# Optimization experiments

Measured on AMD Instinct MI355X. Metric: run time of the kernel, lower is better.

## Reference

```python
import jax, jax.numpy as jnp
import numpy as np

N, K, P, C, H, E, Q, G = 50000, 8, 512, 64, 128, 1600000, 500000, 64

def _gelu(x):
    return jax.nn.gelu(x, approximate=False)  # torch F.gelu default = exact erf

def _mlp(x, Wi, bi, Wh, bh, Wo, bo, Wp=None, bp=None):
    # MLP: lin_in -> gelu -> hid -> (proj skip if in>hidden) -> skip+gelu -> lin_out
    skip = x if Wp is None else x @ Wp.T + bp
    h = _gelu(x @ Wi.T + bi)
    h = h @ Wh.T + bh
    return (skip + _gelu(h)) @ Wo.T + bo

def _sage(x, src, dst, Wl, bl, Wr, n):
    # PyG SAGEConv: mean-aggregate source features at dst, then lin_l(agg)+lin_r(x)
    s = jax.ops.segment_sum(x[src], dst, num_segments=n)
    cnt = jax.ops.segment_sum(jnp.ones((src.shape[0], 1), x.dtype), dst, num_segments=n)
    agg = s / jnp.maximum(cnt, 1.0)
    return agg @ Wl.T + bl + x @ Wr.T

def setup_inputs():
    key = jax.random.key(0)
    ks = iter(jax.random.split(key, 64))
    def lin(o, i):
        return (jax.random.normal(next(ks), (o, i), jnp.float32) / np.sqrt(i)).astype(jnp.float32)
    def bias(o):
        return jnp.zeros((o,), jnp.float32)
    inp = {}
    inp["x"] = jax.random.normal(next(ks), (N, K, P), jnp.float32)
    inp["batch"] = jnp.sort(jax.random.randint(next(ks), (N,), 0, G))
    inp["edge_index"] = jax.random.randint(next(ks), (2, E), 0, N)
    inp["src_idx"] = jax.random.randint(next(ks), (Q,), 0, N)
    inp["dst_idx"] = jax.random.randint(next(ks), (Q,), 0, N)
    # Embedder.mlp : MLP(P, P, H) with proj (P > H)
    inp.update(em_in_W=lin(H, P), em_in_b=bias(H), em_hid_W=lin(H, H), em_hid_b=bias(H),
               em_out_W=lin(P, H), em_out_b=bias(P), em_proj_W=lin(H, P), em_proj_b=bias(H))
    # Embedder.rho : MLP(P, C, H) with proj
    inp.update(rho_in_W=lin(H, P), rho_in_b=bias(H), rho_hid_W=lin(H, H), rho_hid_b=bias(H),
               rho_out_W=lin(C, H), rho_out_b=bias(C), rho_proj_W=lin(H, P), rho_proj_b=bias(H))
    for i in (1, 2, 3):
        inp[f"c{i}_ll_W"] = lin(C, C); inp[f"c{i}_ll_b"] = bias(C); inp[f"c{i}_lr_W"] = lin(C, C)
    # head MLP(3C, 2C, 2C) with proj (3C > 2C)
    inp.update(h1_in_W=lin(H, 3 * C), h1_in_b=bias(H), h1_hid_W=lin(H, H), h1_hid_b=bias(H),
               h1_out_W=lin(2 * C, H), h1_out_b=bias(2 * C), h1_proj_W=lin(H, 3 * C), h1_proj_b=bias(H))
    # head MLP(2C, 1, 2C), no proj
    inp.update(h2_in_W=lin(H, 2 * C), h2_in_b=bias(H), h2_hid_W=lin(H, H), h2_hid_b=bias(H),
               h2_out_W=lin(1, H), h2_out_b=bias(1))
    return inp

def reference(x, batch, edge_index, src_idx, dst_idx,
              em_in_W, em_in_b, em_hid_W, em_hid_b, em_out_W, em_out_b, em_proj_W, em_proj_b,
              rho_in_W, rho_in_b, rho_hid_W, rho_hid_b, rho_out_W, rho_out_b, rho_proj_W, rho_proj_b,
              c1_ll_W, c1_ll_b, c1_lr_W, c2_ll_W, c2_ll_b, c2_lr_W, c3_ll_W, c3_ll_b, c3_lr_W,
              h1_in_W, h1_in_b, h1_hid_W, h1_hid_b, h1_out_W, h1_out_b, h1_proj_W, h1_proj_b,
              h2_in_W, h2_in_b, h2_hid_W, h2_hid_b, h2_out_W, h2_out_b):
    n = x.shape[0]
    # Embedder: per-point MLP, gelu, sum over point-set dim, then rho (dropout = eval identity)
    h = _gelu(_mlp(x, em_in_W, em_in_b, em_hid_W, em_hid_b, em_out_W, em_out_b, em_proj_W, em_proj_b))
    z = _mlp(h.sum(-2), rho_in_W, rho_in_b, rho_hid_W, rho_hid_b, rho_out_W, rho_out_b, rho_proj_W, rho_proj_b)
    src, dst = edge_index[0], edge_index[1]
    z = z + _gelu(_sage(z, src, dst, c1_ll_W, c1_ll_b, c1_lr_W, n))
    z = z + _gelu(_sage(z, src, dst, c2_ll_W, c2_ll_b, c2_lr_W, n))
    z = z + _gelu(_sage(z, src, dst, c3_ll_W, c3_ll_b, c3_lr_W, n))
    node_embeddings = z
    # global_max_pool keyed by batch id, broadcast back via gather
    graph_emb = jax.ops.segment_max(z, batch, num_segments=G)
    ge = graph_emb[batch[src_idx]]  # == graph_emb[batch][src_idx]
    se, de = z[src_idx], z[dst_idx]
    xy = jnp.concatenate([se, de, ge], axis=-1)
    yx = jnp.concatenate([de, se, ge], axis=-1)
    def head(q):
        t = jax.nn.relu(_mlp(q, h1_in_W, h1_in_b, h1_hid_W, h1_hid_b, h1_out_W, h1_out_b, h1_proj_W, h1_proj_b))
        return _mlp(t, h2_in_W, h2_in_b, h2_hid_W, h2_hid_b, h2_out_W, h2_out_b)
    return (node_embeddings, (head(xy), head(yx)), xy)
```

## Files before the change

### kernel.cpp

```cpp
#include <hip/hip_runtime.h>

typedef unsigned short US;
typedef unsigned int   UI;
typedef short  short8 __attribute__((ext_vector_type(8)));
typedef US     u16x8  __attribute__((ext_vector_type(8)));
typedef float  f32x4  __attribute__((ext_vector_type(4)));

#define DEVI __device__ __forceinline__

DEVI float bf2f(US u){ UI i = ((UI)u) << 16; float f; __builtin_memcpy(&f, &i, 4); return f; }
DEVI US f2bf(float x){ UI i; __builtin_memcpy(&i, &x, 4); UI r = (i + 0x7FFFu + ((i >> 16) & 1u)) >> 16; return (US)r; }
DEVI float gelu_f(float x){
    float x2 = x * x;
    float m  = x * fmaf(x2, -0.1029432f, -2.3022052f);
    float e  = __builtin_amdgcn_exp2f(m);
    return x * __builtin_amdgcn_rcpf(1.0f + e);
}
DEVI UI encf(float f){ UI u; __builtin_memcpy(&u, &f, 4); return (u & 0x80000000u) ? ~u : (u | 0x80000000u); }
DEVI float decf(UI u){ UI b = (u & 0x80000000u) ? (u ^ 0x80000000u) : ~u; float f; __builtin_memcpy(&f, &b, 4); return f; }
DEVI int swz(int r, int c, int ld){ int i = r * ld + c; return i ^ ((r & 7) << 3); }

DEVI UI pkbf(float a, float b){ UI u; asm("v_cvt_pk_bf16_f32 %0, %1, %2" : "=v"(u) : "v"(a), "v"(b)); return u; }
DEVI void st4(US* T, int row, int col, float v0, float v1, float v2, float v3){
    uint2 p; p.x = pkbf(v0, v1); p.y = pkbf(v2, v3);
    *(uint2*)&T[swz(row, col, 256)] = p;
}
DEVI void ld4(const US* T, int row, int col, float& v0, float& v1, float& v2, float& v3){
    uint2 q = *(const uint2*)&T[swz(row, col, 256)];
    v0 = bf2f((US)(q.x & 0xffff)); v1 = bf2f((US)(q.x >> 16));
    v2 = bf2f((US)(q.y & 0xffff)); v3 = bf2f((US)(q.y >> 16));
}

enum : int { O_EmW1 = 0, O_EmWh = 131072, O_EmWo = 147456, O_RhoW1 = 212992,
             O_RhoWh = 344064, O_RhoWo = 360448, O_Cat1 = 368640, O_Cat2 = 376832,
             O_Cat3 = 385024, O_H1W1 = 393216, O_H1Wh = 442368, O_H1Wo = 458752,
             O_H2W1 = 475136, O_H2Wh = 491520, W_TOTAL = 507904 };

template<int NT, int NKC, int NTHR, bool SWAP = false>
DEVI void stageWD(const US* __restrict__ Wg, int Kw, const US* __restrict__ A, int lda,
                  int ab0, int ab1, int ab2, int arow0, US* Wb, int tid, f32x4 (&acc)[NT])
{
    const int lane = tid & 63;
    const int wc = (tid >> 6) & 1;
    constexpr int SLAB = NT * 32 * 64;
    #pragma unroll
    for (int n = 0; n < NT; ++n) acc[n] = (f32x4){0.f, 0.f, 0.f, 0.f};
    constexpr int J = (NT * 256) / NTHR;
    u16x8 wreg[J];
    #pragma unroll
    for (int j = 0; j < J; ++j) {
        const int c = tid + NTHR * j;
        wreg[j] = *(const u16x8*)(Wg + (size_t)(c >> 3) * Kw + (c & 7) * 8);
    }
    #pragma unroll
    for (int j = 0; j < J; ++j) {
        const int c = tid + NTHR * j;
        *(u16x8*)&Wb[swz(c >> 3, (c & 7) * 8, 64)] = wreg[j];
    }
    #pragma unroll
    for (int kc = 0; kc < NKC; ++kc) {
        __syncthreads();
        if (kc + 1 < NKC) {
            #pragma unroll
            for (int j = 0; j < J; ++j) {
                const int c = tid + NTHR * j;
                wreg[j] = *(const u16x8*)(Wg + (size_t)(c >> 3) * Kw + (kc + 1) * 64 + (c & 7) * 8);
            }
        }
        const int ab = (kc == 0) ? ab0 : ((kc == 1) ? ab1 : ab2);
        const int bufr = (kc & 1) * SLAB;
        #pragma unroll
        for (int sub = 0; sub < 2; ++sub) {
            const int kk = sub * 32 + ((lane >> 4) << 3);
            short8 a = *(const short8*)&A[swz(arow0 + (lane & 15), ab + kk, lda)];
            #pragma unroll
            for (int n = 0; n < NT; ++n) {
                short8 b = *(const short8*)&Wb[bufr + swz(wc * (NT * 16) + n * 16 + (lane & 15), kk, 64)];
                if (SWAP) acc[n] = __builtin_amdgcn_mfma_f32_16x16x32_bf16(b, a, acc[n], 0, 0, 0);
                else      acc[n] = __builtin_amdgcn_mfma_f32_16x16x32_bf16(a, b, acc[n], 0, 0, 0);
            }
        }
        if (kc + 1 < NKC) {
            const int bufw = ((kc + 1) & 1) * SLAB;
            #pragma unroll
            for (int j = 0; j < J; ++j) {
                const int c = tid + NTHR * j;
                *(u16x8*)&Wb[bufw + swz(c >> 3, (c & 7) * 8, 64)] = wreg[j];
            }
        }
    }
    __syncthreads();
}

template<int NT, int TOTC, int TOTCN, int NKC, bool LAST, bool SWAP>
DEVI void stageWC2(const US* __restrict__ Wg, int Kw, const US* __restrict__ nextWg, int nKw,
                   const US* __restrict__ A, int lda,
                   int aA0, int aA1, int aA2, int aB0, int aB1, int aB2,
                   int arowA, int rofB, int colb,
                   US* Wb, int off0, int off1, int wrN, int tid,
                   f32x4 (&accA)[NT], f32x4 (&accB)[NT])
{
    const int lane = tid & 63;
    const int l15 = lane & 15;
    const int h8 = (lane >> 4) << 3;
    #pragma unroll
    for (int n = 0; n < NT; ++n) {
        accA[n] = (f32x4){0.f, 0.f, 0.f, 0.f};
        accB[n] = (f32x4){0.f, 0.f, 0.f, 0.f};
    }
    constexpr int J  = TOTC  / 128;
    constexpr int JN = TOTCN / 128;
    constexpr int JM = (J > JN) ? J : JN;
    u16x8 wreg[JM];
    #pragma unroll
    for (int kc = 0; kc < NKC; ++kc) {
        __syncthreads();
        if (kc + 1 < NKC) {
            #pragma unroll
            for (int j = 0; j < J; ++j) {
                const int c = tid + 1024 * j;
                wreg[j] = *(const u16x8*)(Wg + (size_t)(c >> 3) * Kw + (kc + 1) * 64 + (c & 7) * 8);
            }
        } else if (!LAST) {
            #pragma unroll
            for (int j = 0; j < JN; ++j) {
                const int c = tid + 1024 * j;
                wreg[j] = *(const u16x8*)(nextWg + (size_t)(c >> 3) * nKw + (c & 7) * 8);
            }
        }
        const int abA = (kc == 0) ? aA0 : ((kc == 1) ? aA1 : aA2);
        const int abB = (kc == 0) ? aB0 : ((kc == 1) ? aB1 : aB2);
        const int rd = (kc & 1) ? off1 : off0;
        #pragma unroll
        for (int sub = 0; sub < 2; ++sub) {
            const int kk = sub * 32 + h8;
            short8 aA = *(const short8*)&A[swz(arowA + l15, abA + kk, lda)];
            short8 aB = *(const short8*)&A[swz(arowA + rofB + l15, abB + kk, lda)];
            #pragma unroll
            for (int n = 0; n < NT; ++n) {
                short8 b = *(const short8*)&Wb[rd + swz(colb + n * 16 + l15, kk, 64)];
                if (SWAP) {
                    accA[n] = __builtin_amdgcn_mfma_f32_16x16x32_bf16(b, aA, accA[n], 0, 0, 0);
                    accB[n] = __builtin_amdgcn_mfma_f32_16x16x32_bf16(b, aB, accB[n], 0, 0, 0);
                } else {
                    accA[n] = __builtin_amdgcn_mfma_f32_16x16x32_bf16(aA, b, accA[n], 0, 0, 0);
                    accB[n] = __builtin_amdgcn_mfma_f32_16x16x32_bf16(aB, b, accB[n], 0, 0, 0);
                }
            }
        }
        if (kc + 1 < NKC) {
            const int wr_ = (kc & 1) ? off0 : off1;
            #pragma unroll
            for (int j = 0; j < J; ++j) {
                const int c = tid + 1024 * j;
                *(u16x8*)&Wb[wr_ + swz(c >> 3, (c & 7) * 8, 64)] = wreg[j];
            }
        } else if (!LAST) {
            #pragma unroll
            for (int j = 0; j < JN; ++j) {
                const int c = tid + 1024 * j;
                *(u16x8*)&Wb[wrN + swz(c >> 3, (c & 7) * 8, 64)] = wreg[j];
            }
        }
    }
    __syncthreads();
}

template<int NT, int NTHR>
DEVI void preloadW(const US* __restrict__ Wg, int Kw, US* Wb, int off, int tid)
{
    constexpr int J = (NT * 256) / NTHR;
    #pragma unroll
    for (int j = 0; j < J; ++j) {
        const int c = tid + NTHR * j;
        u16x8 v = *(const u16x8*)(Wg + (size_t)(c >> 3) * Kw + (c & 7) * 8);
        *(u16x8*)&Wb[off + swz(c >> 3, (c & 7) * 8, 64)] = v;
    }
}

__global__ __launch_bounds__(1024, 4)
void embed_fused(const float* __restrict__ x, const US* __restrict__ WB,
                 const float* __restrict__ b_in, const float* __restrict__ b_proj,
                 const float* __restrict__ b_hid, const float* __restrict__ b_out,
                 US* __restrict__ Ss)
{
    __shared__ __align__(16) US T1[128 * 256];
    __shared__ __align__(16) US Wb[2 * 16384];
    const int tid = threadIdx.x, lane = tid & 63, w = tid >> 6;
    const int wr = w >> 1, wc = w & 1;
    const int h = lane >> 4;
    const int l15 = lane & 15;
    const int grow0 = blockIdx.x * 128;
    const int rowT = wr * 16 + l15;
    const int wr4 = w & 3, cq = w >> 2;
    const int arowA = wr4 * 16;
    const int rA = arowA + l15, rB = rA + 64;

    {
        f32x4 acc[8];
        #pragma unroll
        for (int n = 0; n < 8; ++n) acc[n] = (f32x4){0.f, 0.f, 0.f, 0.f};
        const float* xp = x + (size_t)(grow0 + rowT) * 512 + h * 8;
        float4 pA0, pA1, pA2, pA3, pB0, pB1, pB2, pB3;
        u16x8 wreg[2];
        auto loadW = [&](int kc) {
            #pragma unroll
            for (int j = 0; j < 2; ++j) {
                const int c = tid + 1024 * j;
                wreg[j] = *(const u16x8*)(WB + O_EmW1 + (size_t)(c >> 3) * 512 + kc * 64 + (c & 7) * 8);
            }
        };
        auto writeW = [&](int buf) {
            #pragma unroll
            for (int j = 0; j < 2; ++j) {
                const int c = tid + 1024 * j;
                *(u16x8*)&Wb[buf * 16384 + swz(c >> 3, (c & 7) * 8, 64)] = wreg[j];
            }
        };
        pA0 = *(const float4*)(xp +   0); pA1 = *(const float4*)(xp +   4);
        pA2 = *(const float4*)(xp +  32); pA3 = *(const float4*)(xp +  36);
        loadW(0);
        pB0 = *(const float4*)(xp +  64); pB1 = *(const float4*)(xp +  68);
        pB2 = *(const float4*)(xp +  96); pB3 = *(const float4*)(xp + 100);
        writeW(0);
        #pragma unroll
        for (int k2 = 0; k2 < 4; ++k2) {
            const int kce = 2 * k2, kco = 2 * k2 + 1;
            __syncthreads();
            short8 a0, a1;
            {
                uint4 q;
                q.x = pkbf(pA0.x, pA0.y); q.y = pkbf(pA0.z, pA0.w);
                q.z = pkbf(pA1.x, pA1.y); q.w = pkbf(pA1.z, pA1.w);
                __builtin_memcpy(&a0, &q, 16);
                q.x = pkbf(pA2.x, pA2.y); q.y = pkbf(pA2.z, pA2.w);
                q.z = pkbf(pA3.x, pA3.y); q.w = pkbf(pA3.z, pA3.w);
                __builtin_memcpy(&a1, &q, 16);
            }
            if (kce + 2 < 8) {
                pA0 = *(const float4*)(xp + (kce + 2) * 64);
                pA1 = *(const float4*)(xp + (kce + 2) * 64 + 4);
                pA2 = *(const float4*)(xp + (kce + 2) * 64 + 32);
                pA3 = *(const float4*)(xp + (kce + 2) * 64 + 36);
            }
            loadW(kco);
            #pragma unroll
            for (int n = 0; n < 8; ++n) {
                short8 b = *(const short8*)&Wb[swz(wc * 128 + n * 16 + l15, h * 8, 64)];
                acc[n] = __builtin_amdgcn_mfma_f32_16x16x32_bf16(b, a0, acc[n], 0, 0, 0);
            }
            #pragma unroll
            for (int n = 0; n < 8; ++n) {
                short8 b = *(const short8*)&Wb[swz(wc * 128 + n * 16 + l15, 32 + h * 8, 64)];
                acc[n] = __builtin_amdgcn_mfma_f32_16x16x32_bf16(b, a1, acc[n], 0, 0, 0);
            }
            writeW(1);
            __syncthreads();
            {
                uint4 q;
                q.x = pkbf(pB0.x, pB0.y); q.y = pkbf(pB0.z, pB0.w);
                q.z = pkbf(pB1.x, pB1.y); q.w = pkbf(pB1.z, pB1.w);
                __builtin_memcpy(&a0, &q, 16);
                q.x = pkbf(pB2.x, pB2.y); q.y = pkbf(pB2.z, pB2.w);
                q.z = pkbf(pB3.x, pB3.y); q.w = pkbf(pB3.z, pB3.w);
                __builtin_memcpy(&a1, &q, 16);
            }
            if (kco + 2 < 8) {
                pB0 = *(const float4*)(xp + (kco + 2) * 64);
                pB1 = *(const float4*)(xp + (kco + 2) * 64 + 4);
                pB2 = *(const float4*)(xp + (kco + 2) * 64 + 32);
                pB3 = *(const float4*)(xp + (kco + 2) * 64 + 36);
            }
            u16x8 nx;
            if (kco < 7) loadW(kco + 1);
            else         nx = *(const u16x8*)(WB + O_EmWh + (size_t)(tid >> 3) * 128 + (tid & 7) * 8);
            #pragma unroll
            for (int n = 0; n < 8; ++n) {
                short8 b = *(const short8*)&Wb[16384 + swz(wc * 128 + n * 16 + l15, h * 8, 64)];
                acc[n] = __builtin_amdgcn_mfma_f32_16x16x32_bf16(b, a0, acc[n], 0, 0, 0);
            }
            #pragma unroll
            for (int n = 0; n < 8; ++n) {
                short8 b = *(const short8*)&Wb[16384 + swz(wc * 128 + n * 16 + l15, 32 + h * 8, 64)];
                acc[n] = __builtin_amdgcn_mfma_f32_16x16x32_bf16(b, a1, acc[n], 0, 0, 0);
            }
            if (kco < 7) writeW(0);
            else         *(u16x8*)&Wb[swz(tid >> 3, (tid & 7) * 8, 64)] = nx;
        }
        #pragma unroll
        for (int n = 0; n < 8; ++n) {
            const int col = wc * 128 + n * 16 + h * 4;
            float4 bv = (col < 128) ? *(const float4*)&b_in[col]
                                    : *(const float4*)&b_proj[col - 128];
            float v0 = acc[n][0] + bv.x, v1 = acc[n][1] + bv.y;
            float v2 = acc[n][2] + bv.z, v3 = acc[n][3] + bv.w;
            if (col < 128) { v0 = gelu_f(v0); v1 = gelu_f(v1); v2 = gelu_f(v2); v3 = gelu_f(v3); }
            st4(T1, rowT, col, v0, v1, v2, v3);
        }
    }
    {
        f32x4 accA[2], accB[2];
        stageWC2<2, 128, 256, 2, false, true>(WB + O_EmWh, 128, WB + O_EmWo, 128,
                                              T1, 256, 0, 64, 0, 0, 64, 0,
                                              arowA, 64, cq * 32,
                                              Wb, 0, 8192, 16384, tid, accA, accB);
        #pragma unroll
        for (int n = 0; n < 2; ++n) {
            const int col = cq * 32 + n * 16 + h * 4;
            float4 bv = *(const float4*)&b_hid[col];
            float s0, s1, s2, s3;
            ld4(T1, rA, 128 + col, s0, s1, s2, s3);
            st4(T1, rA, col,
                gelu_f(accA[n][0] + bv.x) + s0, gelu_f(accA[n][1] + bv.y) + s1,
                gelu_f(accA[n][2] + bv.z) + s2, gelu_f(accA[n][3] + bv.w) + s3);
            ld4(T1, rB, 128 + col, s0, s1, s2, s3);
            st4(T1, rB, col,
                gelu_f(accB[n][0] + bv.x) + s0, gelu_f(accB[n][1] + bv.y) + s1,
                gelu_f(accB[n][2] + bv.z) + s2, gelu_f(accB[n][3] + bv.w) + s3);
        }
    }
    #pragma unroll
    for (int p2 = 0; p2 < 2; ++p2) {
        f32x4 accA[4], accB[4];
        if (p2 == 0)
            stageWC2<4, 256, 256, 2, false, false>(WB + O_EmWo, 128, WB + O_EmWo + (size_t)256 * 128, 128,
                                                   T1, 256, 0, 64, 0, 0, 64, 0,
                                                   arowA, 64, cq * 64,
                                                   Wb, 16384, 0, 16384, tid, accA, accB);
        else
            stageWC2<4, 256, 256, 2, true, false>(WB + O_EmWo + (size_t)256 * 128, 128, (const US*)nullptr, 0,
                                                  T1, 256, 0, 64, 0, 0, 64, 0,
                                                  arowA, 64, cq * 64,
                                                  Wb, 16384, 0, 16384, tid, accA, accB);
        #pragma unroll
        for (int n = 0; n < 4; ++n) {
            const int col = cq * 64 + n * 16 + l15;
            const float bv = b_out[p2 * 256 + col];
            float sA = 0.f, sB = 0.f;
            #pragma unroll
            for (int r = 0; r < 4; ++r) { sA += gelu_f(accA[n][r] + bv); sB += gelu_f(accB[n][r] + bv); }
            sA += __shfl_xor(sA, 16);
            sB += __shfl_xor(sB, 16);
            if (((lane >> 4) & 1) == 0) {
                const int nodeA = (grow0 >> 3) + wr4 * 2 + (lane >> 5);
                Ss[(size_t)nodeA * 512 + p2 * 256 + col] = f2bf(sA);
                Ss[(size_t)(nodeA + 8) * 512 + p2 * 256 + col] = f2bf(sB);
            }
        }
    }
}

__global__ __launch_bounds__(512, 2)
void rho_fused(const US* __restrict__ Ss, const US* __restrict__ WB,
               const float* __restrict__ b_in, const float* __restrict__ b_proj,
               const float* __restrict__ b_hid, const float* __restrict__ b_out,
               US* __restrict__ zo, int N)
{
    __shared__ __align__(16) US T1[64 * 256];
    __shared__ __align__(16) US Wb[256 * 64];
    const int tid = threadIdx.x, lane = tid & 63, w = tid >> 6;
    const int wr = w >> 1, wc = w & 1;
    const int h = lane >> 4;
    const int grow0 = blockIdx.x * 64;
    const int rowT = wr * 16 + (lane & 15);

    {
        f32x4 acc[8];
        #pragma unroll
        for (int n = 0; n < 8; ++n) acc[n] = (f32x4){0.f, 0.f, 0.f, 0.f};
        int arow = grow0 + rowT; if (arow >= N) arow = N - 1;
        const US* sp = Ss + (size_t)arow * 512 + h * 8;
        u16x8 a0r, a1r, wreg[4];
        auto loadA = [&](int kc) {
            a0r = *(const u16x8*)(sp + kc * 64);
            a1r = *(const u16x8*)(sp + kc * 64 + 32);
        };
        auto loadW = [&](int kc) {
            #pragma unroll
            for (int j = 0; j < 4; ++j) {
                const int c = tid + 512 * j;
                wreg[j] = *(const u16x8*)(WB + O_RhoW1 + (size_t)(c >> 3) * 512 + kc * 64 + (c & 7) * 8);
            }
        };
        loadA(0); loadW(0);
        for (int kc = 0; kc < 8; ++kc) {
            __syncthreads();
            #pragma unroll
            for (int j = 0; j < 4; ++j) {
                const int c = tid + 512 * j;
                *(u16x8*)&Wb[swz(c >> 3, (c & 7) * 8, 64)] = wreg[j];
            }
            __syncthreads();
            if (kc < 7) loadW(kc + 1);
            short8 a0, a1;
            __builtin_memcpy(&a0, &a0r, 16);
            __builtin_memcpy(&a1, &a1r, 16);
            #pragma unroll
            for (int n = 0; n < 8; ++n) {
                short8 b = *(const short8*)&Wb[swz(wc * 128 + n * 16 + (lane & 15), h * 8, 64)];
                acc[n] = __builtin_amdgcn_mfma_f32_16x16x32_bf16(b, a0, acc[n], 0, 0, 0);
            }
            #pragma unroll
            for (int n = 0; n < 8; ++n) {
                short8 b = *(const short8*)&Wb[swz(wc * 128 + n * 16 + (lane & 15), 32 + h * 8, 64)];
                acc[n] = __builtin_amdgcn_mfma_f32_16x16x32_bf16(b, a1, acc[n], 0, 0, 0);
            }
            if (kc < 7) loadA(kc + 1);
        }
        __syncthreads();
        #pragma unroll
        for (int n = 0; n < 8; ++n) {
            const int col = wc * 128 + n * 16 + h * 4;
            float4 bv = (col < 128) ? *(const float4*)&b_in[col]
                                    : *(const float4*)&b_proj[col - 128];
            float v0 = acc[n][0] + bv.x, v1 = acc[n][1] + bv.y;
            float v2 = acc[n][2] + bv.z, v3 = acc[n][3] + bv.w;
            if (col < 128) { v0 = gelu_f(v0); v1 = gelu_f(v1); v2 = gelu_f(v2); v3 = gelu_f(v3); }
            st4(T1, rowT, col, v0, v1, v2, v3);
        }
    }
    {
        f32x4 acc[4];
        stageWD<4, 2, 512, true>(WB + O_RhoWh, 128, T1, 256, 0, 64, 0, wr * 16, Wb, tid, acc);
        #pragma unroll
        for (int n = 0; n < 4; ++n) {
            const int col = wc * 64 + n * 16 + h * 4;
            float4 bv = *(const float4*)&b_hid[col];
            float s0, s1, s2, s3;
            ld4(T1, rowT, 128 + col, s0, s1, s2, s3);
            st4(T1, rowT, col,
                gelu_f(acc[n][0] + bv.x) + s0, gelu_f(acc[n][1] + bv.y) + s1,
                gelu_f(acc[n][2] + bv.z) + s2, gelu_f(acc[n][3] + bv.w) + s3);
        }
    }
    {
        f32x4 acc[2];
        stageWD<2, 2, 512>(WB + O_RhoWo, 128, T1, 256, 0, 64, 0, wr * 16, Wb, tid, acc);
        #pragma unroll
        for (int n = 0; n < 2; ++n) {
            const int col = wc * 32 + n * 16 + (lane & 15);
            const float bv = b_out[col];
            #pragma unroll
            for (int r = 0; r < 4; ++r) {
                const int node = grow0 + wr * 16 + h * 4 + r;
                if (node < N) zo[(size_t)node * 64 + col] = f2bf(acc[n][r] + bv);
            }
        }
    }
}

__global__ __launch_bounds__(1024, 4)
void head_fused(const int* __restrict__ srcq, const int* __restrict__ dstq,
                const int* __restrict__ batch, const US* __restrict__ z,
                const US* __restrict__ geb, const US* __restrict__ WB,
                const float* __restrict__ b1_in, const float* __restrict__ b1_proj,
                const float* __restrict__ b1_hid, const float* __restrict__ b1_out,
                const float* __restrict__ b2_in, const float* __restrict__ b2_hid,
                const float* __restrict__ w2_out, const float* __restrict__ b2_out,
                float* __restrict__ outH, float* __restrict__ outXY, int Q)
{
    __shared__ __align__(16) US A0[64 * 192];
    __shared__ __align__(16) US T1[128 * 256];
    __shared__ __align__(16) US Wb[2 * 16384];
    __shared__ float wout_s[128];
    const int tid = threadIdx.x, lane = tid & 63, w = tid >> 6;
    const int l15 = lane & 15;
    const int h4 = (lane >> 4) << 2;
    const int q0 = blockIdx.x * 64;
    const int wr4 = w & 3, cq = w >> 2;
    const int arowA = wr4 * 16;
    const int rA = arowA + l15, rB = rA + 64;

    preloadW<8, 1024>(WB + O_H1W1, 192, Wb, 0, tid);

    {
        if (tid < 512) {
            const int r = tid >> 3, hh = tid & 7;
            const int q = q0 + r;
            const int qc = (q < Q) ? q : (Q - 1);
            const int s = srcq[qc], d = dstq[qc];
            const int g = batch[s];
            *(u16x8*)&A0[swz(r, hh * 8, 192)]       = *(const u16x8*)(z + (size_t)s * 64 + hh * 8);
            *(u16x8*)&A0[swz(r, 64 + hh * 8, 192)]  = *(const u16x8*)(z + (size_t)d * 64 + hh * 8);
            *(u16x8*)&A0[swz(r, 128 + hh * 8, 192)] = *(const u16x8*)(geb + (size_t)g * 64 + hh * 8);
        }
        if (tid < 128) wout_s[tid] = w2_out[tid];
    }
    __syncthreads();
    {
        const int row = tid >> 4;
        const int qu  = tid & 15;
        #pragma unroll
        for (int jj = 0; jj < 3; ++jj) {
            const int c4 = (jj * 16 + qu) * 4;
            if (q0 + row < Q) {
                const US* p = &A0[swz(row, c4, 192)];
                float4 o;
                o.x = bf2f(p[0]); o.y = bf2f(p[1]); o.z = bf2f(p[2]); o.w = bf2f(p[3]);
                *(float4*)&outXY[(size_t)(q0 + row) * 192 + c4] = o;
            }
        }
    }
    {
        f32x4 accA[4], accB[4];
        stageWC2<4, 256, 128, 3, false, true>(WB + O_H1W1, 192, WB + O_H1Wh, 128,
                                              A0, 192, 0, 64, 128, 64, 0, 128,
                                              arowA, 0, cq * 64,
                                              Wb, 0, 16384, 16384, tid, accA, accB);
        #pragma unroll
        for (int n = 0; n < 4; ++n) {
            const int col = cq * 64 + n * 16 + h4;
            float4 bv = (col < 128) ? *(const float4*)&b1_in[col]
                                    : *(const float4*)&b1_proj[col - 128];
            float v0 = accA[n][0] + bv.x, v1 = accA[n][1] + bv.y;
            float v2 = accA[n][2] + bv.z, v3 = accA[n][3] + bv.w;
            float u0 = accB[n][0] + bv.x, u1 = accB[n][1] + bv.y;
            float u2 = accB[n][2] + bv.z, u3 = accB[n][3] + bv.w;
            if (col < 128) {
                v0 = gelu_f(v0); v1 = gelu_f(v1); v2 = gelu_f(v2); v3 = gelu_f(v3);
                u0 = gelu_f(u0); u1 = gelu_f(u1); u2 = gelu_f(u2); u3 = gelu_f(u3);
            }
            st4(T1, rA, col, v0, v1, v2, v3);
            st4(T1, rB, col, u0, u1, u2, u3);
        }
    }
    f32x4 accA[2], accB[2];
    const int colb2 = cq * 32;
    stageWC2<2, 128, 128, 2, false, true>(WB + O_H1Wh, 128, WB + O_H1Wo, 128,
                                          T1, 256, 0, 64, 0, 0, 64, 0,
                                          arowA, 64, colb2,
                                          Wb, 16384, 24576, 16384, tid, accA, accB);
    #pragma unroll
    for (int n = 0; n < 2; ++n) {
        const int col = colb2 + n * 16 + h4;
        float4 bv = *(const float4*)&b1_hid[col];
        float s0, s1, s2, s3;
        ld4(T1, rA, 128 + col, s0, s1, s2, s3);
        st4(T1, rA, col,
            gelu_f(accA[n][0] + bv.x) + s0, gelu_f(accA[n][1] + bv.y) + s1,
            gelu_f(accA[n][2] + bv.z) + s2, gelu_f(accA[n][3] + bv.w) + s3);
        ld4(T1, rB, 128 + col, s0, s1, s2, s3);
        st4(T1, rB, col,
            gelu_f(accB[n][0] + bv.x) + s0, gelu_f(accB[n][1] + bv.y) + s1,
            gelu_f(accB[n][2] + bv.z) + s2, gelu_f(accB[n][3] + bv.w) + s3);
    }
    stageWC2<2, 128, 128, 2, false, true>(WB + O_H1Wo, 128, WB + O_H2W1, 128,
                                          T1, 256, 0, 64, 0, 0, 64, 0,
                                          arowA, 64, colb2,
                                          Wb, 16384, 24576, 16384, tid, accA, accB);
    #pragma unroll
    for (int n = 0; n < 2; ++n) {
        const int col = colb2 + n * 16 + h4;
        float4 bv = *(const float4*)&b1_out[col];
        st4(T1, rA, 128 + col,
            fmaxf(accA[n][0] + bv.x, 0.f), fmaxf(accA[n][1] + bv.y, 0.f),
            fmaxf(accA[n][2] + bv.z, 0.f), fmaxf(accA[n][3] + bv.w, 0.f));
        st4(T1, rB, 128 + col,
            fmaxf(accB[n][0] + bv.x, 0.f), fmaxf(accB[n][1] + bv.y, 0.f),
            fmaxf(accB[n][2] + bv.z, 0.f), fmaxf(accB[n][3] + bv.w, 0.f));
    }
    stageWC2<2, 128, 128, 2, false, true>(WB + O_H2W1, 128, WB + O_H2Wh, 128,
                                          T1, 256, 128, 192, 0, 128, 192, 0,
                                          arowA, 64, colb2,
                                          Wb, 16384, 24576, 16384, tid, accA, accB);
    #pragma unroll
    for (int n = 0; n < 2; ++n) {
        const int col = colb2 + n * 16 + h4;
        float4 bv = *(const float4*)&b2_in[col];
        st4(T1, rA, col,
            gelu_f(accA[n][0] + bv.x), gelu_f(accA[n][1] + bv.y),
            gelu_f(accA[n][2] + bv.z), gelu_f(accA[n][3] + bv.w));
        st4(T1, rB, col,
            gelu_f(accB[n][0] + bv.x), gelu_f(accB[n][1] + bv.y),
            gelu_f(accB[n][2] + bv.z), gelu_f(accB[n][3] + bv.w));
    }
    stageWC2<2, 128, 128, 2, true, true>(WB + O_H2Wh, 128, (const US*)nullptr, 0,
                                         T1, 256, 0, 64, 0, 0, 64, 0,
                                         arowA, 64, colb2,
                                         Wb, 16384, 24576, 16384, tid, accA, accB);
    #pragma unroll
    for (int n = 0; n < 2; ++n) {
        const int col = colb2 + n * 16 + h4;
        float4 bv = *(const float4*)&b2_hid[col];
        float t0, t1, t2, t3;
        ld4(T1, rA, 128 + col, t0, t1, t2, t3);
        st4(T1, rA, col,
            gelu_f(accA[n][0] + bv.x) + t0, gelu_f(accA[n][1] + bv.y) + t1,
            gelu_f(accA[n][2] + bv.z) + t2, gelu_f(accA[n][3] + bv.w) + t3);
        ld4(T1, rB, 128 + col, t0, t1, t2, t3);
        st4(T1, rB, col,
            gelu_f(accB[n][0] + bv.x) + t0, gelu_f(accB[n][1] + bv.y) + t1,
            gelu_f(accB[n][2] + bv.z) + t2, gelu_f(accB[n][3] + bv.w) + t3);
    }
    __syncthreads();
    {
        const int r = tid >> 3, hh = tid & 7;
        float a = 0.f;
        u16x8 v0 = *(const u16x8*)&T1[swz(r, hh * 16, 256)];
        u16x8 v1 = *(const u16x8*)&T1[swz(r, hh * 16 + 8, 256)];
        #pragma unroll
        for (int e = 0; e < 8; ++e) {
            a += bf2f(v0[e]) * wout_s[hh * 16 + e];
            a += bf2f(v1[e]) * wout_s[hh * 16 + 8 + e];
        }
        a += __shfl_xor(a, 4);
        a += __shfl_xor(a, 2);
        a += __shfl_xor(a, 1);
        const int q = q0 + (r & 63);
        if ((lane & 7) == 0 && q < Q) outH[(size_t)(r >> 6) * Q + q] = a + b2_out[0];
    }
}

__global__ __launch_bounds__(256, 2)
void sage_gemm(const US* __restrict__ zin, const US* __restrict__ agg,
               const US* __restrict__ Wc, const float* __restrict__ bias,
               US* __restrict__ zout, float* __restrict__ fout, int N)
{
    __shared__ __align__(16) US As[128 * 128];
    __shared__ __align__(16) US Ws[64 * 128];
    const int tid = threadIdx.x, lane = tid & 63, w = tid >> 6;
    const int grow0 = blockIdx.x * 128;
    {
        const int r = tid >> 1, hh = tid & 1;
        int row = grow0 + r; if (row >= N) row = N - 1;
        const US* src = hh ? (zin + (size_t)row * 64) : (agg + (size_t)row * 64);
        #pragma unroll
        for (int j = 0; j < 8; ++j)
            *(u16x8*)&As[swz(r, hh * 64 + 8 * j, 128)] = *(const u16x8*)(src + 8 * j);
    }
    #pragma unroll
    for (int j = 0; j < 4; ++j) {
        const int c = tid + 256 * j;
        *(u16x8*)&Ws[swz(c >> 4, (c & 15) * 8, 128)] =
            *(const u16x8*)(Wc + (size_t)(c >> 4) * 128 + (c & 15) * 8);
    }
    __syncthreads();
    const int rbw = w * 32;
    f32x4 acc[2][4];
    #pragma unroll
    for (int m = 0; m < 2; ++m)
        #pragma unroll
        for (int n = 0; n < 4; ++n) acc[m][n] = (f32x4){0.f, 0.f, 0.f, 0.f};
    #pragma unroll
    for (int kc = 0; kc < 2; ++kc)
        #pragma unroll
        for (int sub = 0; sub < 2; ++sub) {
            const int kk = kc * 64 + sub * 32 + ((lane >> 4) << 3);
            short8 a[2], b[4];
            #pragma unroll
            for (int m = 0; m < 2; ++m) a[m] = *(const short8*)&As[swz(rbw + m * 16 + (lane & 15), kk, 128)];
            #pragma unroll
            for (int n = 0; n < 4; ++n) b[n] = *(const short8*)&Ws[swz(n * 16 + (lane & 15), kk, 128)];
            #pragma unroll
            for (int m = 0; m < 2; ++m)
                #pragma unroll
                for (int n = 0; n < 4; ++n)
                    acc[m][n] = __builtin_amdgcn_mfma_f32_16x16x32_bf16(a[m], b[n], acc[m][n], 0, 0, 0);
        }
    #pragma unroll
    for (int m = 0; m < 2; ++m) {
        const int row0 = rbw + m * 16 + ((lane >> 4) << 2);
        #pragma unroll
        for (int n = 0; n < 4; ++n) {
            const int col = n * 16 + (lane & 15);
            const float bv = bias[col];
            #pragma unroll
            for (int r = 0; r < 4; ++r) {
                const int node = grow0 + row0 + r;
                if (node < N) {
                    const float v = gelu_f(acc[m][n][r] + bv) + bf2f(zin[(size_t)node * 64 + col]);
                    const US bb = f2bf(v);
                    zout[(size_t)node * 64 + col] = bb;
                    if (fout) fout[(size_t)node * 64 + col] = bf2f(bb);
                }
            }
        }
    }
}

struct WSeg { const float* src; int dst; int n; int rl; int ldd; };
struct WPrm { WSeg s[20]; };

__global__ void prep_w(WPrm p, US* __restrict__ wb)
{
    WSeg sg = p.s[blockIdx.x];
    for (int i = threadIdx.x; i < sg.n; i += 256) {
        const int idx = sg.dst + (i / sg.rl) * sg.ldd + (i % sg.rl);
        wb[idx] = f2bf(sg.src[i]);
    }
}

__global__ void count_k(const int* __restrict__ dst, int* __restrict__ cnt, int E)
{
    int e = blockIdx.x * 256 + threadIdx.x;
    if (e < E) atomicAdd(&cnt[dst[e]], 1);
}

__global__ void scan_csr(const int* __restrict__ cnt, int n, int* __restrict__ indp, int* __restrict__ curs)
{
    __shared__ int wsum[16];
    __shared__ int carry_s;
    const int tid = threadIdx.x, lane = tid & 63, w = tid >> 6;
    if (tid == 0) carry_s = 0;
    __syncthreads();
    for (int base = 0; base < n; base += 1024) {
        const int i = base + tid;
        const int v = (i < n) ? cnt[i] : 0;
        int s = v;
        #pragma unroll
        for (int o = 1; o < 64; o <<= 1) { int t = __shfl_up(s, o); if (lane >= o) s += t; }
        if (lane == 63) wsum[w] = s;
        __syncthreads();
        if (w == 0 && lane < 16) {
            int ws2 = wsum[lane];
            #pragma unroll
            for (int o = 1; o < 16; o <<= 1) { int t = __shfl_up(ws2, o); if (lane >= o) ws2 += t; }
            wsum[lane] = ws2;
        }
        __syncthreads();
        const int carry = carry_s;
        const int woff  = (w == 0) ? 0 : wsum[w - 1];
        if (i < n) { const int excl = carry + woff + s - v; indp[i] = excl; curs[i] = excl; }
        __syncthreads();
        if (tid == 0) carry_s = carry + wsum[15];
        __syncthreads();
    }
    if (threadIdx.x == 0) indp[n] = carry_s;
}

__global__ void fill_k(const int* __restrict__ src, const int* __restrict__ dst,
                       int* __restrict__ curs, int* __restrict__ esrc, int E)
{
    int e = blockIdx.x * 256 + threadIdx.x;
    if (e < E) { int p = atomicAdd(&curs[dst[e]], 1); esrc[p] = src[e]; }
}

__global__ void sage_agg(const US* __restrict__ z, const int* __restrict__ indp,
                         const int* __restrict__ esrc, US* __restrict__ agg, int n)
{
    const int w = blockIdx.x * 4 + (threadIdx.x >> 6);
    const int lane = threadIdx.x & 63;
    if (w >= n) return;
    const int beg = indp[w], end = indp[w + 1];
    float acc = 0.f;
    int j = beg;
    for (; j + 4 <= end; j += 4) {
        const int s0 = esrc[j], s1 = esrc[j + 1], s2 = esrc[j + 2], s3 = esrc[j + 3];
        const float v0 = bf2f(z[(size_t)s0 * 64 + lane]);
        const float v1 = bf2f(z[(size_t)s1 * 64 + lane]);
        const float v2 = bf2f(z[(size_t)s2 * 64 + lane]);
        const float v3 = bf2f(z[(size_t)s3 * 64 + lane]);
        acc += (v0 + v1) + (v2 + v3);
    }
    for (; j < end; ++j) acc += bf2f(z[(size_t)esrc[j] * 64 + lane]);
    const float d = (float)(end - beg);
    agg[(size_t)w * 64 + lane] = f2bf(acc / fmaxf(d, 1.0f));
}

__global__ void segmax_k(const US* __restrict__ z, const int* __restrict__ batch,
                         UI* __restrict__ enc, int n, int per)
{
    const int w = blockIdx.x * 4 + (threadIdx.x >> 6);
    const int lane = threadIdx.x & 63;
    const int start = w * per;
    if (start >= n) return;
    const int end = (start + per < n) ? start + per : n;
    int g = batch[start];
    float m = -3.0e38f;
    for (int i = start; i < end; ++i) {
        const int b = batch[i];
        if (b != g) { atomicMax(&enc[(size_t)g * 64 + lane], encf(m)); g = b; m = -3.0e38f; }
        m = fmaxf(m, bf2f(z[(size_t)i * 64 + lane]));
    }
    atomicMax(&enc[(size_t)g * 64 + lane], encf(m));
}

__global__ void decode_ge(const UI* __restrict__ enc, US* __restrict__ geb)
{
    const int i = blockIdx.x * 256 + threadIdx.x;
    if (i < 4096) geb[i] = f2bf(decf(enc[i]));
}

extern "C" void kernel_launch(void* const* d_in, const int* in_sizes, int n_in,
                              void* d_out, int out_size, void* d_ws, size_t ws_size,
                              hipStream_t stream)
{
    (void)in_sizes; (void)n_in; (void)out_size; (void)ws_size;

    const float* x      = (const float*)d_in[0];
    const int*   batch  = (const int*)d_in[1];
    const int*   eidx   = (const int*)d_in[2];
    const int*   srcq   = (const int*)d_in[3];
    const int*   dstq   = (const int*)d_in[4];
    const float* em_in_b   = (const float*)d_in[6];
    const float* em_hid_b  = (const float*)d_in[8];
    const float* em_out_b  = (const float*)d_in[10];
    const float* em_proj_b = (const float*)d_in[12];
    const float* rho_in_b  = (const float*)d_in[14];
    const float* rho_hid_b = (const float*)d_in[16];
    const float* rho_out_b = (const float*)d_in[18];
    const float* rho_proj_b= (const float*)d_in[20];
    const float* c_ll_W[3] = {(const float*)d_in[21], (const float*)d_in[24], (const float*)d_in[27]};
    const float* c_ll_b[3] = {(const float*)d_in[22], (const float*)d_in[25], (const float*)d_in[28]};
    const float* c_lr_W[3] = {(const float*)d_in[23], (const float*)d_in[26], (const float*)d_in[29]};
    const float* h1_in_b   = (const float*)d_in[31];
    const float* h1_hid_b  = (const float*)d_in[33];
    const float* h1_out_b  = (const float*)d_in[35];
    const float* h1_proj_b = (const float*)d_in[37];
    const float* h2_in_b   = (const float*)d_in[39];
    const float* h2_hid_b  = (const float*)d_in[41];
    const float* h2_out_W  = (const float*)d_in[42];
    const float* h2_out_b  = (const float*)d_in[43];

    const int N = 50000, E = 1600000, Q = 500000;
    float* out = (float*)d_out;

    char* wsb = (char*)d_ws;
    size_t off = 0;
    auto ALLOC = [&](size_t bytes) -> char* {
        char* p = wsb + off; off = (off + bytes + 255) & ~(size_t)255; return p;
    };
    US*  WB   = (US*)ALLOC((size_t)W_TOTAL * 2);
    US*  Ss   = (US*)ALLOC((size_t)N * 512 * 2);
    US*  z0   = (US*)ALLOC((size_t)N * 64 * 2);
    US*  z1   = (US*)ALLOC((size_t)N * 64 * 2);
    US*  aggB = (US*)ALLOC((size_t)N * 64 * 2);
    int* cnt  = (int*)ALLOC((size_t)N * 4);
    int* indp = (int*)ALLOC((size_t)(N + 1) * 4);
    int* curs = (int*)ALLOC((size_t)N * 4);
    int* esrc = (int*)ALLOC((size_t)E * 4);
    UI*  enc  = (UI*)ALLOC(4096 * 4);
    US*  geb  = (US*)ALLOC(4096 * 2);

    const int catOff[3] = {O_Cat1, O_Cat2, O_Cat3};

    WPrm pw; int si = 0;
    auto SEG = [&](const float* s, int o, int n, int rl, int ldd) {
        pw.s[si].src = s; pw.s[si].dst = o; pw.s[si].n = n; pw.s[si].rl = rl; pw.s[si].ldd = ldd; ++si;
    };
    SEG((const float*)d_in[5],  O_EmW1,          65536, 65536, 65536);
    SEG((const float*)d_in[11], O_EmW1 + 65536,  65536, 65536, 65536);
    SEG((const float*)d_in[7],  O_EmWh,          16384, 16384, 16384);
    SEG((const float*)d_in[9],  O_EmWo,          65536, 65536, 65536);
    SEG((const float*)d_in[13], O_RhoW1,         65536, 65536, 65536);
    SEG((const float*)d_in[19], O_RhoW1 + 65536, 65536, 65536, 65536);
    SEG((const float*)d_in[15], O_RhoWh,         16384, 16384, 16384);
    SEG((const float*)d_in[17], O_RhoWo,          8192,  8192,  8192);
    for (int i = 0; i < 3; ++i) {
        SEG(c_ll_W[i], catOff[i],      4096, 64, 128);
        SEG(c_lr_W[i], catOff[i] + 64, 4096, 64, 128);
    }
    SEG((const float*)d_in[30], O_H1W1,          24576, 24576, 24576);
    SEG((const float*)d_in[36], O_H1W1 + 24576,  24576, 24576, 24576);
    SEG((const float*)d_in[32], O_H1Wh,          16384, 16384, 16384);
    SEG((const float*)d_in[34], O_H1Wo,          16384, 16384, 16384);
    SEG((const float*)d_in[38], O_H2W1,          16384, 16384, 16384);
    SEG((const float*)d_in[40], O_H2Wh,          16384, 16384, 16384);
    prep_w<<<dim3(20), dim3(256), 0, stream>>>(pw, WB);

    hipMemsetAsync(cnt, 0, (size_t)N * 4, stream);
    count_k<<<dim3((E + 255) / 256), dim3(256), 0, stream>>>(eidx + E, cnt, E);
    scan_csr<<<dim3(1), dim3(1024), 0, stream>>>(cnt, N, indp, curs);
    fill_k<<<dim3((E + 255) / 256), dim3(256), 0, stream>>>(eidx, eidx + E, curs, esrc, E);

    embed_fused<<<dim3(3125), dim3(1024), 0, stream>>>(x, WB, em_in_b, em_proj_b, em_hid_b, em_out_b, Ss);
    rho_fused<<<dim3((N + 63) / 64), dim3(512), 0, stream>>>(Ss, WB, rho_in_b, rho_proj_b, rho_hid_b, rho_out_b, z0, N);

    US* zin = z0; US* zout = z1;
    for (int ci = 0; ci < 3; ++ci) {
        sage_agg<<<dim3((N + 3) / 4), dim3(256), 0, stream>>>(zin, indp, esrc, aggB, N);
        sage_gemm<<<dim3((N + 127) / 128), dim3(256), 0, stream>>>(
            zin, aggB, WB + catOff[ci], c_ll_b[ci], zout,
            (ci == 2) ? out : (float*)nullptr, N);
        US* t = zin; zin = zout; zout = t;
    }
    US* zf = zin;

    hipMemsetAsync(enc, 0, 4096 * 4, stream);
    segmax_k<<<dim3((N + 511) / 512), dim3(256), 0, stream>>>(zf, batch, enc, N, 128);
    decode_ge<<<dim3(16), dim3(256), 0, stream>>>(enc, geb);

    head_fused<<<dim3((Q + 63) / 64), dim3(1024), 0, stream>>>(
        srcq, dstq, batch, zf, geb, WB,
        h1_in_b, h1_proj_b, h1_hid_b, h1_out_b, h2_in_b, h2_hid_b, h2_out_W, h2_out_b,
        out + (size_t)N * 64, out + (size_t)N * 64 + 2 * (size_t)Q, Q);
}
```

Before: 1.456 ms.

## Fuse SAGE mean aggregation into sage_gemm and retile embed first GEMM

The separate sage_agg kernel is removed. Each sage_gemm block now gathers neighbour features through the CSR and computes the mean directly into its shared A tile, and reuses the staged z row for the residual instead of rereading global memory. This drops three kernel launches and the aggB round trip, but only 392 blocks of 256 threads now do the irregular gather, so latency hiding may be worse. Separately, the embed first GEMM is restructured so each wave computes two 16-row tiles against 64 output columns with a single-stage-per-iteration double buffer, so each B fragment read from shared memory feeds two MFMAs.

```diff
diff --git a/kernel.cpp b/kernel.cpp
--- a/kernel.cpp
+++ b/kernel.cpp
@@ -18,7 +18,7 @@
 }
 DEVI UI encf(float f){ UI u; __builtin_memcpy(&u, &f, 4); return (u & 0x80000000u) ? ~u : (u | 0x80000000u); }
 DEVI float decf(UI u){ UI b = (u & 0x80000000u) ? (u ^ 0x80000000u) : ~u; float f; __builtin_memcpy(&f, &b, 4); return f; }
-DEVI int swz(int r, int c, int ld){ int i = r * ld + c; return i ^ ((r & 7) << 3); }
+DEVI int swz(int r, int c, int ld){ int i = r * ld + c; return i ^ (((r) & 7) << 3); }
 
 DEVI UI pkbf(float a, float b){ UI u; asm("v_cvt_pk_bf16_f32 %0, %1, %2" : "=v"(u) : "v"(a), "v"(b)); return u; }
 DEVI void st4(US* T, int row, int col, float v0, float v1, float v2, float v3){
@@ -187,22 +187,30 @@
     __shared__ __align__(16) US T1[128 * 256];
     __shared__ __align__(16) US Wb[2 * 16384];
     const int tid = threadIdx.x, lane = tid & 63, w = tid >> 6;
-    const int wr = w >> 1, wc = w & 1;
     const int h = lane >> 4;
     const int l15 = lane & 15;
     const int grow0 = blockIdx.x * 128;
-    const int rowT = wr * 16 + l15;
     const int wr4 = w & 3, cq = w >> 2;
     const int arowA = wr4 * 16;
     const int rA = arowA + l15, rB = rA + 64;
 
     {
-        f32x4 acc[8];
-        #pragma unroll
-        for (int n = 0; n < 8; ++n) acc[n] = (f32x4){0.f, 0.f, 0.f, 0.f};
-        const float* xp = x + (size_t)(grow0 + rowT) * 512 + h * 8;
-        float4 pA0, pA1, pA2, pA3, pB0, pB1, pB2, pB3;
+        f32x4 accA[4], accB[4];
+        #pragma unroll
+        for (int n = 0; n < 4; ++n) {
+            accA[n] = (f32x4){0.f, 0.f, 0.f, 0.f};
+            accB[n] = (f32x4){0.f, 0.f, 0.f, 0.f};
+        }
+        const float* xpA = x + (size_t)(grow0 + rA) * 512 + h * 8;
+        const float* xpB = x + (size_t)(grow0 + rB) * 512 + h * 8;
+        float4 aa0, aa1, aa2, aa3, bb0, bb1, bb2, bb3;
         u16x8 wreg[2];
+        auto loadA = [&](int kc) {
+            aa0 = *(const float4*)(xpA + kc * 64);      aa1 = *(const float4*)(xpA + kc * 64 + 4);
+            aa2 = *(const float4*)(xpA + kc * 64 + 32); aa3 = *(const float4*)(xpA + kc * 64 + 36);
+            bb0 = *(const float4*)(xpB + kc * 64);      bb1 = *(const float4*)(xpB + kc * 64 + 4);
+            bb2 = *(const float4*)(xpB + kc * 64 + 32); bb3 = *(const float4*)(xpB + kc * 64 + 36);
+        };
         auto loadW = [&](int kc) {
             #pragma unroll
             for (int j = 0; j < 2; ++j) {
@@ -217,85 +225,60 @@
                 *(u16x8*)&Wb[buf * 16384 + swz(c >> 3, (c & 7) * 8, 64)] = wreg[j];
             }
         };
-        pA0 = *(const float4*)(xp +   0); pA1 = *(const float4*)(xp +   4);
-        pA2 = *(const float4*)(xp +  32); pA3 = *(const float4*)(xp +  36);
-        loadW(0);
-        pB0 = *(const float4*)(xp +  64); pB1 = *(const float4*)(xp +  68);
-        pB2 = *(const float4*)(xp +  96); pB3 = *(const float4*)(xp + 100);
-        writeW(0);
-        #pragma unroll
-        for (int k2 = 0; k2 < 4; ++k2) {
-            const int kce = 2 * k2, kco = 2 * k2 + 1;
+        loadA(0); loadW(0); writeW(0);
+        #pragma unroll
+        for (int kc = 0; kc < 8; ++kc) {
             __syncthreads();
-            short8 a0, a1;
+            short8 a0A, a1A, a0B, a1B;
             {
                 uint4 q;
-                q.x = pkbf(pA0.x, pA0.y); q.y = pkbf(pA0.z, pA0.w);
-                q.z = pkbf(pA1.x, pA1.y); q.w = pkbf(pA1.z, pA1.w);
-                __builtin_memcpy(&a0, &q, 16);
-                q.x = pkbf(pA2.x, pA2.y); q.y = pkbf(pA2.z, pA2.w);
-                q.z = pkbf(pA3.x, pA3.y); q.w = pkbf(pA3.z, pA3.w);
-                __builtin_memcpy(&a1, &q, 16);
-            }
-            if (kce + 2 < 8) {
-                pA0 = *(const float4*)(xp + (kce + 2) * 64);
-                pA1 = *(const float4*)(xp + (kce + 2) * 64 + 4);
-                pA2 = *(const float4*)(xp + (kce + 2) * 64 + 32);
-                pA3 = *(const float4*)(xp + (kce + 2) * 64 + 36);
-            }
-            loadW(kco);
-            #pragma unroll
-            for (int n = 0; n < 8; ++n) {
-                short8 b = *(const short8*)&Wb[swz(wc * 128 + n * 16 + l15, h * 8, 64)];
-                acc[n] = __builtin_amdgcn_mfma_f32_16x16x32_bf16(b, a0, acc[n], 0, 0, 0);
-            }
-            #pragma unroll
-            for (int n = 0; n < 8; ++n) {
-                short8 b = *(const short8*)&Wb[swz(wc * 128 + n * 16 + l15, 32 + h * 8, 64)];
-                acc[n] = __builtin_amdgcn_mfma_f32_16x16x32_bf16(b, a1, acc[n], 0, 0, 0);
-            }
-            writeW(1);
-            __syncthreads();
-            {
-                uint4 q;
-                q.x = pkbf(pB0.x, pB0.y); q.y = pkbf(pB0.z, pB0.w);
-                q.z = pkbf(pB1.x, pB1.y); q.w = pkbf(pB1.z, pB1.w);
-                __builtin_memcpy(&a0, &q, 16);
-                q.x = pkbf(pB2.x, pB2.y); q.y = pkbf(pB2.z, pB2.w);
-                q.z = pkbf(pB3.x, pB3.y); q.w = pkbf(pB3.z, pB3.w);
-                __builtin_memcpy(&a1, &q, 16);
-            }
-            if (kco + 2 < 8) {
-                pB0 = *(const float4*)(xp + (kco + 2) * 64);
-                pB1 = *(const float4*)(xp + (kco + 2) * 64 + 4);
-                pB2 = *(const float4*)(xp + (kco + 2) * 64 + 32);
-                pB3 = *(const float4*)(xp + (kco + 2) * 64 + 36);
+                q.x = pkbf(aa0.x, aa0.y); q.y = pkbf(aa0.z, aa0.w);
+                q.z = pkbf(aa1.x, aa1.y); q.w = pkbf(aa1.z, aa1.w);
+                __builtin_memcpy(&a0A, &q, 16);
+                q.x = pkbf(aa2.x, aa2.y); q.y = pkbf(aa2.z, aa2.w);
+                q.z = pkbf(aa3.x, aa3.y); q.w = pkbf(aa3.z, aa3.w);
+                __builtin_memcpy(&a1A, &q, 16);
+                q.x = pkbf(bb0.x, bb0.y); q.y = pkbf(bb0.z, bb0.w);
+                q.z = pkbf(bb1.x, bb1.y); q.w = pkbf(bb1.z, bb1.w);
+                __builtin_memcpy(&a0B, &q, 16);
+                q.x = pkbf(bb2.x, bb2.y); q.y = pkbf(bb2.z, bb2.w);
+                q.z = pkbf(bb3.x, bb3.y); q.w = pkbf(bb3.z, bb3.w);
+                __builtin_memcpy(&a1B, &q, 16);
             }
             u16x8 nx;
-            if (kco < 7) loadW(kco + 1);
-            else         nx = *(const u16x8*)(WB + O_EmWh + (size_t)(tid >> 3) * 128 + (tid & 7) * 8);
-            #pragma unroll
-            for (int n = 0; n < 8; ++n) {
-                short8 b = *(const short8*)&Wb[16384 + swz(wc * 128 + n * 16 + l15, h * 8, 64)];
-                acc[n] = __builtin_amdgcn_mfma_f32_16x16x32_bf16(b, a0, acc[n], 0, 0, 0);
-            }
-            #pragma unroll
-            for (int n = 0; n < 8; ++n) {
-                short8 b = *(const short8*)&Wb[16384 + swz(wc * 128 + n * 16 + l15, 32 + h * 8, 64)];
-                acc[n] = __builtin_amdgcn_mfma_f32_16x16x32_bf16(b, a1, acc[n], 0, 0, 0);
-            }
-            if (kco < 7) writeW(0);
-            else         *(u16x8*)&Wb[swz(tid >> 3, (tid & 7) * 8, 64)] = nx;
-        }
-        #pragma unroll
-        for (int n = 0; n < 8; ++n) {
-            const int col = wc * 128 + n * 16 + h * 4;
+            if (kc < 7) { loadA(kc + 1); loadW(kc + 1); }
+            else        { nx = *(const u16x8*)(WB + O_EmWh + (size_t)(tid >> 3) * 128 + (tid & 7) * 8); }
+            const int bufr = (kc & 1) * 16384;
+            #pragma unroll
+            for (int n = 0; n < 4; ++n) {
+                short8 b = *(const short8*)&Wb[bufr + swz(cq * 64 + n * 16 + l15, h * 8, 64)];
+                accA[n] = __builtin_amdgcn_mfma_f32_16x16x32_bf16(b, a0A, accA[n], 0, 0, 0);
+                accB[n] = __builtin_amdgcn_mfma_f32_16x16x32_bf16(b, a0B, accB[n], 0, 0, 0);
+            }
+            #pragma unroll
+            for (int n = 0; n < 4; ++n) {
+                short8 b = *(const short8*)&Wb[bufr + swz(cq * 64 + n * 16 + l15, 32 + h * 8, 64)];
+                accA[n] = __builtin_amdgcn_mfma_f32_16x16x32_bf16(b, a1A, accA[n], 0, 0, 0);
+                accB[n] = __builtin_amdgcn_mfma_f32_16x16x32_bf16(b, a1B, accB[n], 0, 0, 0);
+            }
+            if (kc < 7) writeW((kc + 1) & 1);
+            else        *(u16x8*)&Wb[swz(tid >> 3, (tid & 7) * 8, 64)] = nx;
+        }
+        #pragma unroll
+        for (int n = 0; n < 4; ++n) {
+            const int col = cq * 64 + n * 16 + h * 4;
             float4 bv = (col < 128) ? *(const float4*)&b_in[col]
                                     : *(const float4*)&b_proj[col - 128];
-            float v0 = acc[n][0] + bv.x, v1 = acc[n][1] + bv.y;
-            float v2 = acc[n][2] + bv.z, v3 = acc[n][3] + bv.w;
-            if (col < 128) { v0 = gelu_f(v0); v1 = gelu_f(v1); v2 = gelu_f(v2); v3 = gelu_f(v3); }
-            st4(T1, rowT, col, v0, v1, v2, v3);
+            float v0 = accA[n][0] + bv.x, v1 = accA[n][1] + bv.y;
+            float v2 = accA[n][2] + bv.z, v3 = accA[n][3] + bv.w;
+            float u0 = accB[n][0] + bv.x, u1 = accB[n][1] + bv.y;
+            float u2 = accB[n][2] + bv.z, u3 = accB[n][3] + bv.w;
+            if (col < 128) {
+                v0 = gelu_f(v0); v1 = gelu_f(v1); v2 = gelu_f(v2); v3 = gelu_f(v3);
+                u0 = gelu_f(u0); u1 = gelu_f(u1); u2 = gelu_f(u2); u3 = gelu_f(u3);
+            }
+            st4(T1, rA, col, v0, v1, v2, v3);
+            st4(T1, rB, col, u0, u1, u2, u3);
         }
     }
     {
@@ -612,7 +595,8 @@
 }
 
 __global__ __launch_bounds__(256, 2)
-void sage_gemm(const US* __restrict__ zin, const US* __restrict__ agg,
+void sage_gemm(const US* __restrict__ zin, const int* __restrict__ indp,
+               const int* __restrict__ esrc,
                const US* __restrict__ Wc, const float* __restrict__ bias,
                US* __restrict__ zout, float* __restrict__ fout, int N)
 {
@@ -620,20 +604,36 @@
     __shared__ __align__(16) US Ws[64 * 128];
     const int tid = threadIdx.x, lane = tid & 63, w = tid >> 6;
     const int grow0 = blockIdx.x * 128;
-    {
-        const int r = tid >> 1, hh = tid & 1;
-        int row = grow0 + r; if (row >= N) row = N - 1;
-        const US* src = hh ? (zin + (size_t)row * 64) : (agg + (size_t)row * 64);
-        #pragma unroll
-        for (int j = 0; j < 8; ++j)
-            *(u16x8*)&As[swz(r, hh * 64 + 8 * j, 128)] = *(const u16x8*)(src + 8 * j);
-    }
     #pragma unroll
     for (int j = 0; j < 4; ++j) {
         const int c = tid + 256 * j;
         *(u16x8*)&Ws[swz(c >> 4, (c & 15) * 8, 128)] =
             *(const u16x8*)(Wc + (size_t)(c >> 4) * 128 + (c & 15) * 8);
     }
+    for (int i = 0; i < 32; ++i) {
+        const int r = w * 32 + i;
+        const int node = grow0 + r;
+        float acc = 0.f;
+        US zv = 0;
+        float dv = 1.f;
+        if (node < N) {
+            const int beg = indp[node], end = indp[node + 1];
+            int j = beg;
+            for (; j + 4 <= end; j += 4) {
+                const int s0 = esrc[j], s1 = esrc[j + 1], s2 = esrc[j + 2], s3 = esrc[j + 3];
+                const float v0 = bf2f(zin[(size_t)s0 * 64 + lane]);
+                const float v1 = bf2f(zin[(size_t)s1 * 64 + lane]);
+                const float v2 = bf2f(zin[(size_t)s2 * 64 + lane]);
+                const float v3 = bf2f(zin[(size_t)s3 * 64 + lane]);
+                acc += (v0 + v1) + (v2 + v3);
+            }
+            for (; j < end; ++j) acc += bf2f(zin[(size_t)esrc[j] * 64 + lane]);
+            dv = fmaxf((float)(end - beg), 1.0f);
+            zv = zin[(size_t)node * 64 + lane];
+        }
+        As[swz(r, lane, 128)] = f2bf(acc / dv);
+        As[swz(r, 64 + lane, 128)] = zv;
+    }
     __syncthreads();
     const int rbw = w * 32;
     f32x4 acc[2][4];
@@ -668,7 +668,8 @@
             for (int r = 0; r < 4; ++r) {
                 const int node = grow0 + row0 + r;
                 if (node < N) {
-                    const float v = gelu_f(acc[m][n][r] + bv) + bf2f(zin[(size_t)node * 64 + col]);
+                    const float zr = bf2f(As[swz(row0 + r, 64 + col, 128)]);
+                    const float v = gelu_f(acc[m][n][r] + bv) + zr;
                     const US bb = f2bf(v);
                     zout[(size_t)node * 64 + col] = bb;
                     if (fout) fout[(size_t)node * 64 + col] = bf2f(bb);
@@ -733,28 +734,6 @@
 {
     int e = blockIdx.x * 256 + threadIdx.x;
     if (e < E) { int p = atomicAdd(&curs[dst[e]], 1); esrc[p] = src[e]; }
-}
-
-__global__ void sage_agg(const US* __restrict__ z, const int* __restrict__ indp,
-                         const int* __restrict__ esrc, US* __restrict__ agg, int n)
-{
-    const int w = blockIdx.x * 4 + (threadIdx.x >> 6);
-    const int lane = threadIdx.x & 63;
-    if (w >= n) return;
-    const int beg = indp[w], end = indp[w + 1];
-    float acc = 0.f;
-    int j = beg;
-    for (; j + 4 <= end; j += 4) {
-        const int s0 = esrc[j], s1 = esrc[j + 1], s2 = esrc[j + 2], s3 = esrc[j + 3];
-        const float v0 = bf2f(z[(size_t)s0 * 64 + lane]);
-        const float v1 = bf2f(z[(size_t)s1 * 64 + lane]);
-        const float v2 = bf2f(z[(size_t)s2 * 64 + lane]);
-        const float v3 = bf2f(z[(size_t)s3 * 64 + lane]);
-        acc += (v0 + v1) + (v2 + v3);
-    }
-    for (; j < end; ++j) acc += bf2f(z[(size_t)esrc[j] * 64 + lane]);
-    const float d = (float)(end - beg);
-    agg[(size_t)w * 64 + lane] = f2bf(acc / fmaxf(d, 1.0f));
 }
 
 __global__ void segmax_k(const US* __restrict__ z, const int* __restrict__ batch,
@@ -824,7 +803,6 @@
     US*  Ss   = (US*)ALLOC((size_t)N * 512 * 2);
     US*  z0   = (US*)ALLOC((size_t)N * 64 * 2);
     US*  z1   = (US*)ALLOC((size_t)N * 64 * 2);
-    US*  aggB = (US*)ALLOC((size_t)N * 64 * 2);
     int* cnt  = (int*)ALLOC((size_t)N * 4);
     int* indp = (int*)ALLOC((size_t)(N + 1) * 4);
     int* curs = (int*)ALLOC((size_t)N * 4);
@@ -868,9 +846,8 @@
 
     US* zin = z0; US* zout = z1;
     for (int ci = 0; ci < 3; ++ci) {
-        sage_agg<<<dim3((N + 3) / 4), dim3(256), 0, stream>>>(zin, indp, esrc, aggB, N);
         sage_gemm<<<dim3((N + 127) / 128), dim3(256), 0, stream>>>(
-            zin, aggB, WB + catOff[ci], c_ll_b[ci], zout,
+            zin, indp, esrc, WB + catOff[ci], c_ll_b[ci], zout,
             (ci == 2) ? out : (float*)nullptr, N);
         US* t = zin; zin = zout; zout = t;
     }
```

Measured after the change: 2.044 ms. 40.4% more time.
